# Kernel optimization log

Measured on AMD Instinct MI355X. Metric: run time of the kernel, lower is better.

The kernel has to match this reference:

```python
import jax, jax.numpy as jnp
import numpy as np

HIDDEN = 2048
N_HEADS = 32
N_KV = 8
HEAD_DIM = 64
ROPE_THETA = 10000.0


def setup_inputs() -> dict:
    key = jax.random.key(0)
    k0, k1, k2, k3, k4 = jax.random.split(key, 5)
    B, S = 2, 2048
    scale_in = 1.0 / np.sqrt(HIDDEN)
    return {
        "hidden_states": jax.random.normal(k0, (B, S, HIDDEN), dtype=jnp.float32),
        # weights stored [in, out] (transpose of torch Linear.weight)
        "Wq": jax.random.normal(k1, (HIDDEN, N_HEADS * HEAD_DIM), dtype=jnp.float32) * scale_in,
        "Wk": jax.random.normal(k2, (HIDDEN, N_KV * HEAD_DIM), dtype=jnp.float32) * scale_in,
        "Wv": jax.random.normal(k3, (HIDDEN, N_KV * HEAD_DIM), dtype=jnp.float32) * scale_in,
        "Wo": jax.random.normal(k4, (N_HEADS * HEAD_DIM, HIDDEN), dtype=jnp.float32) * scale_in,
    }


def _rope_tables(seq_len, dim, theta):
    inv_freq = 1.0 / (theta ** (jnp.arange(0, dim, 2, dtype=jnp.float32) / dim))
    t = jnp.arange(seq_len, dtype=jnp.float32)
    freqs = jnp.outer(t, inv_freq)              # [S, D/2]
    emb = jnp.concatenate([freqs, freqs], -1)   # [S, D]
    return jnp.cos(emb), jnp.sin(emb)


def _rotate_half(x):
    d = x.shape[-1] // 2
    return jnp.concatenate([-x[..., d:], x[..., :d]], axis=-1)


def reference(hidden_states, Wq, Wk, Wv, Wo):
    B, S, _ = hidden_states.shape
    G = N_HEADS // N_KV  # groups per kv head

    q = (hidden_states @ Wq).reshape(B, S, N_HEADS, HEAD_DIM).transpose(0, 2, 1, 3)  # [B,H,S,D]
    k = (hidden_states @ Wk).reshape(B, S, N_KV, HEAD_DIM).transpose(0, 2, 1, 3)     # [B,KV,S,D]
    v = (hidden_states @ Wv).reshape(B, S, N_KV, HEAD_DIM).transpose(0, 2, 1, 3)

    cos, sin = _rope_tables(S, HEAD_DIM, ROPE_THETA)  # [S,D]
    q = q * cos + _rotate_half(q) * sin
    k = k * cos + _rotate_half(k) * sin

    # GQA without materializing repeated KV: fold q heads into [KV, G]
    qg = q.reshape(B, N_KV, G, S, HEAD_DIM)
    scale = HEAD_DIM ** -0.5
    scores = jnp.einsum("bkgsd,bktd->bkgst", qg, k) * scale  # [B,KV,G,S,S]

    causal = jnp.tril(jnp.ones((S, S), dtype=bool))
    scores = jnp.where(causal, scores, jnp.float32(-1e30))
    probs = jax.nn.softmax(scores, axis=-1)

    out = jnp.einsum("bkgst,bktd->bkgsd", probs, v)          # [B,KV,G,S,D]
    out = out.reshape(B, N_HEADS, S, HEAD_DIM).transpose(0, 2, 1, 3).reshape(B, S, N_HEADS * HEAD_DIM)
    return out @ Wo
```

## Files before the change

### kernel.cpp

```cpp
#include <hip/hip_runtime.h>
#include <cstdint>
#include <cstddef>

typedef __attribute__((ext_vector_type(8))) short short8;
typedef __attribute__((ext_vector_type(4))) float f32x4;
typedef __attribute__((ext_vector_type(16))) float f32x16;

#define MFMA16(a, b, c) __builtin_amdgcn_mfma_f32_16x16x32_bf16((a), (b), (c), 0, 0, 0)
#define MFMA32(a, b, c) __builtin_amdgcn_mfma_f32_32x32x16_bf16((a), (b), (c), 0, 0, 0)

union F2U { float f; unsigned int u; };
union U4S8 { uint4 u4; unsigned short s[8]; short8 v; };

__device__ __forceinline__ unsigned short f2bf(float f) {
  F2U x; x.f = f;
  unsigned int r = x.u + 0x7fffu + ((x.u >> 16) & 1u);
  return (unsigned short)(r >> 16);
}
__device__ __forceinline__ float bf2f(unsigned short s) {
  F2U x; x.u = ((unsigned int)s) << 16;
  return x.f;
}
__device__ __forceinline__ float fexp2(float x) {
  float r; asm("v_exp_f32 %0, %1" : "=v"(r) : "v"(x)); return r;
}
__device__ __forceinline__ unsigned int cvtpk(float lo, float hiv) {
  unsigned int r; asm("v_cvt_pk_bf16_f32 %0, %1, %2" : "=v"(r) : "v"(lo), "v"(hiv)); return r;
}

#define HIDDEN 2048
#define NHEADS 32
#define NKV 8
#define HDIM 64
#define SEQ 2048
#define BATCH 2
#define NTOK (BATCH * SEQ)
#define QKVN 3072
#define QSCALE 0.18033688011117309f

__global__ __launch_bounds__(256) void rope_table_kernel(float* __restrict__ ct, float* __restrict__ st) {
  int idx = blockIdx.x * 256 + threadIdx.x;
  int s = idx >> 5;
  int i = idx & 31;
  float invf = expf(-(float)i * (9.210340371976184f / 32.0f));
  float f = (float)s * invf;
  ct[idx] = cosf(f);
  st[idx] = sinf(f);
}

__global__ __launch_bounds__(256) void convert_x_kernel(const float* __restrict__ X,
                                                        unsigned short* __restrict__ Xb) {
  size_t i = ((size_t)blockIdx.x * 256 + threadIdx.x) * 8;
  float4 a0 = *(const float4*)(X + i);
  float4 a1 = *(const float4*)(X + i + 4);
  U4S8 p;
  p.s[0] = f2bf(a0.x); p.s[1] = f2bf(a0.y); p.s[2] = f2bf(a0.z); p.s[3] = f2bf(a0.w);
  p.s[4] = f2bf(a1.x); p.s[5] = f2bf(a1.y); p.s[6] = f2bf(a1.z); p.s[7] = f2bf(a1.w);
  *(short8*)(Xb + i) = p.v;
}

__global__ __launch_bounds__(256) void transpose_w_kernel(const float* __restrict__ W,
                                                          unsigned short* __restrict__ Wt,
                                                          int N, int row_off) {
  __shared__ unsigned short lt[64][72];
  const int t = threadIdx.x;
  const int k0 = blockIdx.y * 64, n0 = blockIdx.x * 64;
  #pragma unroll
  for (int p = 0; p < 4; ++p) {
    int kr = p * 16 + (t >> 4);
    int nc = (t & 15) * 4;
    float4 v = *(const float4*)&W[(size_t)(k0 + kr) * N + n0 + nc];
    lt[nc + 0][kr] = f2bf(v.x);
    lt[nc + 1][kr] = f2bf(v.y);
    lt[nc + 2][kr] = f2bf(v.z);
    lt[nc + 3][kr] = f2bf(v.w);
  }
  __syncthreads();
  #pragma unroll
  for (int p = 0; p < 2; ++p) {
    int nr = p * 32 + (t >> 3);
    int kc = (t & 7) * 8;
    *(short8*)&Wt[(size_t)(row_off + n0 + nr) * HIDDEN + k0 + kc] = *(const short8*)&lt[nr][kc];
  }
}

template<int MODE>
__global__ __launch_bounds__(256) void gemm128_kernel(const unsigned short* __restrict__ Ab,
                                                      const unsigned short* __restrict__ Bt,
                                                      void* __restrict__ Cp,
                                                      int M, int N, int K,
                                                      const float* __restrict__ ct,
                                                      const float* __restrict__ st) {
  __shared__ __align__(16) unsigned short lds_a[128][64];
  __shared__ __align__(16) unsigned short lds_b[128][64];

  const int t = threadIdx.x, lane = t & 63, w = t >> 6;
  const int lr = lane & 15, lh = lane >> 4;

  const int orig = blockIdx.y * gridDim.x + blockIdx.x;
  const int nwg  = (int)(gridDim.x * gridDim.y);
  const int cpx  = nwg >> 3;
  const int swz  = (orig & 7) * cpx + (orig >> 3);
  const int m0 = (swz / (int)gridDim.x) * 128;
  const int n0 = (swz % (int)gridDim.x) * 128;

  const int wr = (w >> 1) * 64, wc = (w & 1) * 64;

  f32x4 acc[4][4] = {};

  for (int k0 = 0; k0 < K; k0 += 64) {
    __syncthreads();
    #pragma unroll
    for (int c = 0; c < 4; ++c) {
      int row = w * 32 + c * 8 + (lane >> 3);
      int cks = (lane & 7) ^ (row & 7);
      __builtin_amdgcn_global_load_lds(
          (const __attribute__((address_space(1))) unsigned int*)(Ab + (size_t)(m0 + row) * K + k0 + cks * 8),
          (__attribute__((address_space(3))) unsigned int*)&lds_a[w * 32 + c * 8][0], 16, 0, 0);
      __builtin_amdgcn_global_load_lds(
          (const __attribute__((address_space(1))) unsigned int*)(Bt + (size_t)(n0 + row) * K + k0 + cks * 8),
          (__attribute__((address_space(3))) unsigned int*)&lds_b[w * 32 + c * 8][0], 16, 0, 0);
    }
    __syncthreads();

    #pragma unroll
    for (int kk = 0; kk < 2; ++kk) {
      short8 af[4], bf[4];
      #pragma unroll
      for (int i = 0; i < 4; ++i) {
        int row = wr + i * 16 + lr;
        af[i] = *(const short8*)((const char*)&lds_a[0][0] + row * 128 + (((kk * 4 + lh) ^ (row & 7)) * 16));
      }
      #pragma unroll
      for (int j = 0; j < 4; ++j) {
        int row = wc + j * 16 + lr;
        bf[j] = *(const short8*)((const char*)&lds_b[0][0] + row * 128 + (((kk * 4 + lh) ^ (row & 7)) * 16));
      }
      #pragma unroll
      for (int i = 0; i < 4; ++i)
        #pragma unroll
        for (int j = 0; j < 4; ++j)
          acc[i][j] = MFMA16(af[i], bf[j], acc[i][j]);
    }
  }

  if constexpr (MODE == 0) {
    #pragma unroll
    for (int i = 0; i < 4; ++i)
      #pragma unroll
      for (int j = 0; j < 4; ++j)
        #pragma unroll
        for (int r = 0; r < 4; ++r) {
          int row = m0 + wr + i * 16 + lh * 4 + r;
          int col = n0 + wc + j * 16 + lr;
          ((float*)Cp)[(size_t)row * N + col] = acc[i][j][r];
        }
  } else {
    const bool isV = (n0 >= 2560);
    const bool isQ = (n0 < 2048);
    #pragma unroll
    for (int i = 0; i < 4; ++i)
      #pragma unroll
      for (int r = 0; r < 4; ++r) {
        int row = m0 + wr + i * 16 + lh * 4 + r;
        int s_tok = row & (SEQ - 1);
        float c0 = 0.f, s0 = 0.f, c1 = 0.f, s1 = 0.f;
        if (!isV) {
          c0 = ct[s_tok * 32 + lr];      s0 = st[s_tok * 32 + lr];
          c1 = ct[s_tok * 32 + 16 + lr]; s1 = st[s_tok * 32 + 16 + lr];
        }
        #pragma unroll
        for (int j = 0; j < 4; ++j) {
          int col = n0 + wc + j * 16 + lr;
          float v = acc[i][j][r];
          float o;
          if (isV) {
            o = v;
          } else {
            float p = acc[i][j ^ 2][r];
            float cc = (j & 1) ? c1 : c0;
            float ss = (j & 1) ? s1 : s0;
            o = v * cc + ((j & 2) ? p : -p) * ss;
            if (isQ) o *= QSCALE;
          }
          ((unsigned short*)Cp)[(size_t)row * N + col] = f2bf(o);
        }
      }
  }
}

__global__ __launch_bounds__(256) void v_pack_kernel(const unsigned short* __restrict__ QKV,
                                                     unsigned short* __restrict__ Vt) {
  int idx = blockIdx.x * 256 + threadIdx.x;
  int m = idx >> 9;
  int c = idx & 511;
  int b = m >> 11, s = m & 2047;
  int kv = c >> 6, d = c & 63;
  Vt[(((size_t)(b * NKV + kv)) * HDIM + d) * SEQ + s] = QKV[(size_t)m * QKVN + 2560 + c];
}

#define KVBLK 64

__global__ __launch_bounds__(256, 4) void flash_kernel(const unsigned short* __restrict__ QKV,
                                                       const unsigned short* __restrict__ Vt,
                                                       unsigned short* __restrict__ Ob) {
  const int bx = blockIdx.x;
  const int h = blockIdx.y;
  const int b = blockIdx.z;
  const int kv = h >> 2;
  const int t = threadIdx.x;
  const int lane = t & 63;
  const int w = t >> 6;
  const int q = lane & 31;
  const int hi = lane >> 5;

  __shared__ __align__(16) char smem[32768];
  unsigned short* Klds = (unsigned short*)smem;
  unsigned short* Vlds = (unsigned short*)(smem + 16384);

  const unsigned short* Kg = QKV + (size_t)b * SEQ * QKVN + 2048 + kv * 64;
  const unsigned short* Vg = Vt + ((size_t)(b * NKV + kv)) * HDIM * SEQ;
  const unsigned short* Qh = QKV + (size_t)b * SEQ * QKVN + h * 64;

  const int srow = w * 16 + (lane >> 3);
  const int scks = (lane & 7) ^ (srow & 7);
  const unsigned short* Ksrc = Kg + (size_t)srow * QKVN + scks * 8;
  const unsigned short* Vsrc = Vg + (size_t)srow * SEQ + scks * 8;

  #define STAGE_KV(buf, kt0)                                                              \
    do {                                                                                  \
      __builtin_amdgcn_global_load_lds(                                                   \
          (const __attribute__((address_space(1))) unsigned int*)(Ksrc + (size_t)(kt0) * QKVN), \
          (__attribute__((address_space(3))) unsigned int*)(Klds + (buf) * 4096 + w * 1024), 16, 0, 0); \
      __builtin_amdgcn_global_load_lds(                                                   \
          (const __attribute__((address_space(1))) unsigned int*)(Ksrc + (size_t)(kt0) * QKVN + 8 * QKVN), \
          (__attribute__((address_space(3))) unsigned int*)(Klds + (buf) * 4096 + w * 1024 + 512), 16, 0, 0); \
      __builtin_amdgcn_global_load_lds(                                                   \
          (const __attribute__((address_space(1))) unsigned int*)(Vsrc + (kt0)),          \
          (__attribute__((address_space(3))) unsigned int*)(Vlds + (buf) * 4096 + w * 1024), 16, 0, 0); \
      __builtin_amdgcn_global_load_lds(                                                   \
          (const __attribute__((address_space(1))) unsigned int*)(Vsrc + (kt0) + 8 * SEQ), \
          (__attribute__((address_space(3))) unsigned int*)(Vlds + (buf) * 4096 + w * 1024 + 512), 16, 0, 0); \
    } while (0)

  #pragma unroll 1
  for (int seg = 0; seg < 2; ++seg) {
    const int qb = seg ? bx : (15 - bx);
    const int wq0 = qb * 128 + w * 32;

    short8 qf[4];
    #pragma unroll
    for (int f = 0; f < 4; ++f)
      qf[f] = *(const short8*)&Qh[(size_t)(wq0 + q) * QKVN + f * 16 + hi * 8];

    f32x16 o0 = {}, o1 = {};
    float m_run = -1e30f, l_run = 0.f;

    const int nt_blk = qb * 2 + 2;
    const int nt_w   = qb * 2 + (w >> 1) + 1;

    __syncthreads();
    STAGE_KV(0, 0);
    __syncthreads();
    int cur = 0;

    for (int tt = 0; tt < nt_blk; ++tt) {
      if (tt + 1 < nt_blk) STAGE_KV(cur ^ 1, (tt + 1) * KVBLK);

      if (tt < nt_w) {
        const int kt0 = tt * KVBLK;
        const unsigned short* Kt = Klds + cur * 4096;
        const unsigned short* Vl = Vlds + cur * 4096;

        #pragma unroll
        for (int hk = 0; hk < 2; ++hk) {
          const int kbase = kt0 + hk * 32;
          if (kbase <= wq0 + 31) {
            f32x16 s = {};
            __builtin_amdgcn_s_setprio(1);
            #pragma unroll
            for (int f = 0; f < 4; ++f) {
              short8 kf = *(const short8*)(Kt + (hk * 32 + q) * 64 + (((f * 2 + hi) ^ (q & 7)) * 8));
              s = MFMA32(kf, qf[f], s);
            }
            __builtin_amdgcn_s_setprio(0);

            if (kbase + 31 > wq0) {
              #pragma unroll
              for (int r = 0; r < 16; ++r) {
                int kl = (r & 3) + 8 * (r >> 2) + 4 * hi;
                if (kbase + kl > wq0 + q) s[r] = -1e30f;
              }
            }

            float mt = -1e30f;
            #pragma unroll
            for (int r = 0; r < 16; ++r) mt = fmaxf(mt, s[r]);
            mt = fmaxf(mt, __shfl_xor(mt, 32, 64));

            const bool resc = __any(mt > m_run + 11.0f);
            if (resc) {
              float mn = fmaxf(m_run, mt);
              float alpha = fexp2(m_run - mn);
              m_run = mn;
              l_run *= alpha;
              #pragma unroll
              for (int r = 0; r < 16; ++r) { o0[r] *= alpha; o1[r] *= alpha; }
            }
            float ls = 0.f;
            #pragma unroll
            for (int r = 0; r < 16; ++r) {
              float p = fexp2(s[r] - m_run);
              s[r] = p;
              ls += p;
            }
            ls += __shfl_xor(ls, 32, 64);
            l_run += ls;

            unsigned int own[8], rcv[8];
            #pragma unroll
            for (int g = 0; g < 8; ++g)
              own[g] = cvtpk(s[2 * g], s[2 * g + 1]);
            #pragma unroll
            for (int g = 0; g < 8; ++g)
              rcv[g] = (unsigned int)__shfl_xor((int)own[g], 32, 64);

            __builtin_amdgcn_s_setprio(1);
            {
              U4S8 pfv;
              pfv.u4.x = hi ? rcv[2] : own[0];
              pfv.u4.y = hi ? rcv[3] : own[1];
              pfv.u4.z = hi ? own[2] : rcv[0];
              pfv.u4.w = hi ? own[3] : rcv[1];
              int co = ((hk * 4 + hi) ^ (q & 7)) * 8;
              short8 vf0 = *(const short8*)(Vl + q * 64 + co);
              short8 vf1 = *(const short8*)(Vl + (32 + q) * 64 + co);
              o0 = MFMA32(vf0, pfv.v, o0);
              o1 = MFMA32(vf1, pfv.v, o1);
            }
            {
              U4S8 pfv;
              pfv.u4.x = hi ? rcv[6] : own[4];
              pfv.u4.y = hi ? rcv[7] : own[5];
              pfv.u4.z = hi ? own[6] : rcv[4];
              pfv.u4.w = hi ? own[7] : rcv[5];
              int co = ((hk * 4 + 2 + hi) ^ (q & 7)) * 8;
              short8 vf0 = *(const short8*)(Vl + q * 64 + co);
              short8 vf1 = *(const short8*)(Vl + (32 + q) * 64 + co);
              o0 = MFMA32(vf0, pfv.v, o0);
              o1 = MFMA32(vf1, pfv.v, o1);
            }
            __builtin_amdgcn_s_setprio(0);
          }
        }
      }

      __syncthreads();
      cur ^= 1;
    }

    unsigned short* lo = (unsigned short*)smem + (size_t)w * 32 * 72;
    float inv = 1.0f / l_run;
    #pragma unroll
    for (int gg = 0; gg < 8; ++gg) {
      int r = 2 * gg;
      int dl = (r & 3) + 8 * (r >> 2) + 4 * hi;
      unsigned int w0 = (unsigned int)f2bf(o0[r] * inv) | ((unsigned int)f2bf(o0[r + 1] * inv) << 16);
      unsigned int w1 = (unsigned int)f2bf(o1[r] * inv) | ((unsigned int)f2bf(o1[r + 1] * inv) << 16);
      *(unsigned int*)&lo[q * 72 + dl] = w0;
      *(unsigned int*)&lo[q * 72 + 32 + dl] = w1;
    }
    {
      int row = lane >> 1;
      int ch = (lane & 1) * 32;
      uint4 x0 = *(const uint4*)&lo[row * 72 + ch + 0];
      uint4 x1 = *(const uint4*)&lo[row * 72 + ch + 8];
      uint4 x2 = *(const uint4*)&lo[row * 72 + ch + 16];
      uint4 x3 = *(const uint4*)&lo[row * 72 + ch + 24];
      unsigned short* dst = &Ob[(size_t)(b * SEQ + wq0 + row) * (NHEADS * HDIM) + h * HDIM + ch];
      *(uint4*)(dst + 0)  = x0;
      *(uint4*)(dst + 8)  = x1;
      *(uint4*)(dst + 16) = x2;
      *(uint4*)(dst + 24) = x3;
    }
  }
}

extern "C" void kernel_launch(void* const* d_in, const int* in_sizes, int n_in,
                              void* d_out, int out_size, void* d_ws, size_t ws_size,
                              hipStream_t stream) {
  const float* X  = (const float*)d_in[0];
  const float* Wq = (const float*)d_in[1];
  const float* Wk = (const float*)d_in[2];
  const float* Wv = (const float*)d_in[3];
  const float* Wo = (const float*)d_in[4];
  float* out = (float*)d_out;

  char* ws = (char*)d_ws;
  size_t off = 0;
  auto carve = [&](size_t bytes) -> void* {
    void* p = ws + off;
    off += (bytes + 255) & ~(size_t)255;
    return p;
  };
  float* rope_cos = (float*)carve((size_t)SEQ * 32 * 4);
  float* rope_sin = (float*)carve((size_t)SEQ * 32 * 4);
  unsigned short* Xb     = (unsigned short*)carve((size_t)NTOK * HIDDEN * 2);
  unsigned short* Wqkv_t = (unsigned short*)carve((size_t)QKVN * HIDDEN * 2);
  unsigned short* Wot    = (unsigned short*)carve((size_t)HIDDEN * HIDDEN * 2);
  unsigned short* QKVb   = (unsigned short*)carve((size_t)NTOK * QKVN * 2);
  unsigned short* Vt     = (unsigned short*)carve((size_t)BATCH * NKV * HDIM * SEQ * 2);
  unsigned short* Ob     = Xb;

  rope_table_kernel<<<dim3(256), dim3(256), 0, stream>>>(rope_cos, rope_sin);
  convert_x_kernel<<<dim3((NTOK * HIDDEN) / (256 * 8)), dim3(256), 0, stream>>>(X, Xb);

  transpose_w_kernel<<<dim3(2048 / 64, HIDDEN / 64), dim3(256), 0, stream>>>(Wq, Wqkv_t, 2048, 0);
  transpose_w_kernel<<<dim3(512 / 64,  HIDDEN / 64), dim3(256), 0, stream>>>(Wk, Wqkv_t, 512, 2048);
  transpose_w_kernel<<<dim3(512 / 64,  HIDDEN / 64), dim3(256), 0, stream>>>(Wv, Wqkv_t, 512, 2560);
  transpose_w_kernel<<<dim3(2048 / 64, HIDDEN / 64), dim3(256), 0, stream>>>(Wo, Wot, 2048, 0);

  gemm128_kernel<1><<<dim3(QKVN / 128, NTOK / 128), dim3(256), 0, stream>>>(
      Xb, Wqkv_t, QKVb, NTOK, QKVN, HIDDEN, rope_cos, rope_sin);

  v_pack_kernel<<<dim3((NTOK * NKV * HDIM) / 256), dim3(256), 0, stream>>>(QKVb, Vt);

  flash_kernel<<<dim3(8, NHEADS, BATCH), dim3(256), 0, stream>>>(QKVb, Vt, Ob);

  gemm128_kernel<0><<<dim3(HIDDEN / 128, NTOK / 128), dim3(256), 0, stream>>>(
      Ob, Wot, out, NTOK, HIDDEN, HIDDEN, nullptr, nullptr);
}
```

Before: 226.0 us.

## Split KV tiles across wave pairs in flash kernel and merge partial softmax

The flash attention block grows from 4 to 8 waves. Each pair of waves shares a 32-row query slice, and each wave of the pair handles one 32-key half of every 64-key tile. Partial max, sum and output accumulators are combined through shared memory at the end. This doubles the waves working on the same KV staging, aiming to raise occupancy and hide latency within the causal attention loop. In exchange it adds an LDS reduction step with extra barriers and a larger block, and launch_bounds(512,4) may tighten the register limit.

Result: no change. 222.3 us (-1.6%).

```diff
diff --git a/kernel.cpp b/kernel.cpp
--- a/kernel.cpp
+++ b/kernel.cpp
@@ -201,7 +201,7 @@
 
 #define KVBLK 64
 
-__global__ __launch_bounds__(256, 4) void flash_kernel(const unsigned short* __restrict__ QKV,
+__global__ __launch_bounds__(512, 4) void flash_kernel(const unsigned short* __restrict__ QKV,
                                                        const unsigned short* __restrict__ Vt,
                                                        unsigned short* __restrict__ Ob) {
   const int bx = blockIdx.x;
@@ -211,18 +211,21 @@
   const int t = threadIdx.x;
   const int lane = t & 63;
   const int w = t >> 6;
+  const int p = w >> 1;
+  const int kh = w & 1;
   const int q = lane & 31;
   const int hi = lane >> 5;
 
-  __shared__ __align__(16) char smem[32768];
+  __shared__ __align__(16) char smem[34816];
   unsigned short* Klds = (unsigned short*)smem;
   unsigned short* Vlds = (unsigned short*)(smem + 16384);
+  float* mlArea = (float*)(smem + 32768);
 
   const unsigned short* Kg = QKV + (size_t)b * SEQ * QKVN + 2048 + kv * 64;
   const unsigned short* Vg = Vt + ((size_t)(b * NKV + kv)) * HDIM * SEQ;
   const unsigned short* Qh = QKV + (size_t)b * SEQ * QKVN + h * 64;
 
-  const int srow = w * 16 + (lane >> 3);
+  const int srow = w * 8 + (lane >> 3);
   const int scks = (lane & 7) ^ (srow & 7);
   const unsigned short* Ksrc = Kg + (size_t)srow * QKVN + scks * 8;
   const unsigned short* Vsrc = Vg + (size_t)srow * SEQ + scks * 8;
@@ -231,22 +234,16 @@
     do {                                                                                  \
       __builtin_amdgcn_global_load_lds(                                                   \
           (const __attribute__((address_space(1))) unsigned int*)(Ksrc + (size_t)(kt0) * QKVN), \
-          (__attribute__((address_space(3))) unsigned int*)(Klds + (buf) * 4096 + w * 1024), 16, 0, 0); \
-      __builtin_amdgcn_global_load_lds(                                                   \
-          (const __attribute__((address_space(1))) unsigned int*)(Ksrc + (size_t)(kt0) * QKVN + 8 * QKVN), \
-          (__attribute__((address_space(3))) unsigned int*)(Klds + (buf) * 4096 + w * 1024 + 512), 16, 0, 0); \
+          (__attribute__((address_space(3))) unsigned int*)(Klds + (buf) * 4096 + w * 512), 16, 0, 0); \
       __builtin_amdgcn_global_load_lds(                                                   \
           (const __attribute__((address_space(1))) unsigned int*)(Vsrc + (kt0)),          \
-          (__attribute__((address_space(3))) unsigned int*)(Vlds + (buf) * 4096 + w * 1024), 16, 0, 0); \
-      __builtin_amdgcn_global_load_lds(                                                   \
-          (const __attribute__((address_space(1))) unsigned int*)(Vsrc + (kt0) + 8 * SEQ), \
-          (__attribute__((address_space(3))) unsigned int*)(Vlds + (buf) * 4096 + w * 1024 + 512), 16, 0, 0); \
+          (__attribute__((address_space(3))) unsigned int*)(Vlds + (buf) * 4096 + w * 512), 16, 0, 0); \
     } while (0)
 
   #pragma unroll 1
   for (int seg = 0; seg < 2; ++seg) {
     const int qb = seg ? bx : (15 - bx);
-    const int wq0 = qb * 128 + w * 32;
+    const int wq0 = qb * 128 + p * 32;
 
     short8 qf[4];
     #pragma unroll
@@ -257,7 +254,6 @@
     float m_run = -1e30f, l_run = 0.f;
 
     const int nt_blk = qb * 2 + 2;
-    const int nt_w   = qb * 2 + (w >> 1) + 1;
 
     __syncthreads();
     STAGE_KV(0, 0);
@@ -267,121 +263,145 @@
     for (int tt = 0; tt < nt_blk; ++tt) {
       if (tt + 1 < nt_blk) STAGE_KV(cur ^ 1, (tt + 1) * KVBLK);
 
-      if (tt < nt_w) {
-        const int kt0 = tt * KVBLK;
+      const int kbase = tt * KVBLK + kh * 32;
+      if (kbase <= wq0 + 31) {
         const unsigned short* Kt = Klds + cur * 4096;
         const unsigned short* Vl = Vlds + cur * 4096;
 
-        #pragma unroll
-        for (int hk = 0; hk < 2; ++hk) {
-          const int kbase = kt0 + hk * 32;
-          if (kbase <= wq0 + 31) {
-            f32x16 s = {};
-            __builtin_amdgcn_s_setprio(1);
-            #pragma unroll
-            for (int f = 0; f < 4; ++f) {
-              short8 kf = *(const short8*)(Kt + (hk * 32 + q) * 64 + (((f * 2 + hi) ^ (q & 7)) * 8));
-              s = MFMA32(kf, qf[f], s);
-            }
-            __builtin_amdgcn_s_setprio(0);
-
-            if (kbase + 31 > wq0) {
-              #pragma unroll
-              for (int r = 0; r < 16; ++r) {
-                int kl = (r & 3) + 8 * (r >> 2) + 4 * hi;
-                if (kbase + kl > wq0 + q) s[r] = -1e30f;
-              }
-            }
-
-            float mt = -1e30f;
-            #pragma unroll
-            for (int r = 0; r < 16; ++r) mt = fmaxf(mt, s[r]);
-            mt = fmaxf(mt, __shfl_xor(mt, 32, 64));
-
-            const bool resc = __any(mt > m_run + 11.0f);
-            if (resc) {
-              float mn = fmaxf(m_run, mt);
-              float alpha = fexp2(m_run - mn);
-              m_run = mn;
-              l_run *= alpha;
-              #pragma unroll
-              for (int r = 0; r < 16; ++r) { o0[r] *= alpha; o1[r] *= alpha; }
-            }
-            float ls = 0.f;
-            #pragma unroll
-            for (int r = 0; r < 16; ++r) {
-              float p = fexp2(s[r] - m_run);
-              s[r] = p;
-              ls += p;
-            }
-            ls += __shfl_xor(ls, 32, 64);
-            l_run += ls;
-
-            unsigned int own[8], rcv[8];
-            #pragma unroll
-            for (int g = 0; g < 8; ++g)
-              own[g] = cvtpk(s[2 * g], s[2 * g + 1]);
-            #pragma unroll
-            for (int g = 0; g < 8; ++g)
-              rcv[g] = (unsigned int)__shfl_xor((int)own[g], 32, 64);
-
-            __builtin_amdgcn_s_setprio(1);
-            {
-              U4S8 pfv;
-              pfv.u4.x = hi ? rcv[2] : own[0];
-              pfv.u4.y = hi ? rcv[3] : own[1];
-              pfv.u4.z = hi ? own[2] : rcv[0];
-              pfv.u4.w = hi ? own[3] : rcv[1];
-              int co = ((hk * 4 + hi) ^ (q & 7)) * 8;
-              short8 vf0 = *(const short8*)(Vl + q * 64 + co);
-              short8 vf1 = *(const short8*)(Vl + (32 + q) * 64 + co);
-              o0 = MFMA32(vf0, pfv.v, o0);
-              o1 = MFMA32(vf1, pfv.v, o1);
-            }
-            {
-              U4S8 pfv;
-              pfv.u4.x = hi ? rcv[6] : own[4];
-              pfv.u4.y = hi ? rcv[7] : own[5];
-              pfv.u4.z = hi ? own[6] : rcv[4];
-              pfv.u4.w = hi ? own[7] : rcv[5];
-              int co = ((hk * 4 + 2 + hi) ^ (q & 7)) * 8;
-              short8 vf0 = *(const short8*)(Vl + q * 64 + co);
-              short8 vf1 = *(const short8*)(Vl + (32 + q) * 64 + co);
-              o0 = MFMA32(vf0, pfv.v, o0);
-              o1 = MFMA32(vf1, pfv.v, o1);
-            }
-            __builtin_amdgcn_s_setprio(0);
+        f32x16 s = {};
+        __builtin_amdgcn_s_setprio(1);
+        #pragma unroll
+        for (int f = 0; f < 4; ++f) {
+          short8 kf = *(const short8*)(Kt + (kh * 32 + q) * 64 + (((f * 2 + hi) ^ (q & 7)) * 8));
+          s = MFMA32(kf, qf[f], s);
+        }
+        __builtin_amdgcn_s_setprio(0);
+
+        if (kbase + 31 > wq0) {
+          #pragma unroll
+          for (int r = 0; r < 16; ++r) {
+            int kl = (r & 3) + 8 * (r >> 2) + 4 * hi;
+            if (kbase + kl > wq0 + q) s[r] = -1e30f;
           }
         }
+
+        float mt = -1e30f;
+        #pragma unroll
+        for (int r = 0; r < 16; ++r) mt = fmaxf(mt, s[r]);
+        mt = fmaxf(mt, __shfl_xor(mt, 32, 64));
+
+        const bool resc = __any(mt > m_run + 11.0f);
+        if (resc) {
+          float mn = fmaxf(m_run, mt);
+          float alpha = fexp2(m_run - mn);
+          m_run = mn;
+          l_run *= alpha;
+          #pragma unroll
+          for (int r = 0; r < 16; ++r) { o0[r] *= alpha; o1[r] *= alpha; }
+        }
+        float ls = 0.f;
+        #pragma unroll
+        for (int r = 0; r < 16; ++r) {
+          float pp = fexp2(s[r] - m_run);
+          s[r] = pp;
+          ls += pp;
+        }
+        ls += __shfl_xor(ls, 32, 64);
+        l_run += ls;
+
+        unsigned int own[8], rcv[8];
+        #pragma unroll
+        for (int g = 0; g < 8; ++g)
+          own[g] = cvtpk(s[2 * g], s[2 * g + 1]);
+        #pragma unroll
+        for (int g = 0; g < 8; ++g)
+          rcv[g] = (unsigned int)__shfl_xor((int)own[g], 32, 64);
+
+        __builtin_amdgcn_s_setprio(1);
+        {
+          U4S8 pfv;
+          pfv.u4.x = hi ? rcv[2] : own[0];
+          pfv.u4.y = hi ? rcv[3] : own[1];
+          pfv.u4.z = hi ? own[2] : rcv[0];
+          pfv.u4.w = hi ? own[3] : rcv[1];
+          int co = ((kh * 4 + hi) ^ (q & 7)) * 8;
+          short8 vf0 = *(const short8*)(Vl + q * 64 + co);
+          short8 vf1 = *(const short8*)(Vl + (32 + q) * 64 + co);
+          o0 = MFMA32(vf0, pfv.v, o0);
+          o1 = MFMA32(vf1, pfv.v, o1);
+        }
+        {
+          U4S8 pfv;
+          pfv.u4.x = hi ? rcv[6] : own[4];
+          pfv.u4.y = hi ? rcv[7] : own[5];
+          pfv.u4.z = hi ? own[6] : rcv[4];
+          pfv.u4.w = hi ? own[7] : rcv[5];
+          int co = ((kh * 4 + 2 + hi) ^ (q & 7)) * 8;
+          short8 vf0 = *(const short8*)(Vl + q * 64 + co);
+          short8 vf1 = *(const short8*)(Vl + (32 + q) * 64 + co);
+          o0 = MFMA32(vf0, pfv.v, o0);
+          o1 = MFMA32(vf1, pfv.v, o1);
+        }
+        __builtin_amdgcn_s_setprio(0);
       }
 
       __syncthreads();
       cur ^= 1;
     }
 
-    unsigned short* lo = (unsigned short*)smem + (size_t)w * 32 * 72;
-    float inv = 1.0f / l_run;
-    #pragma unroll
-    for (int gg = 0; gg < 8; ++gg) {
-      int r = 2 * gg;
-      int dl = (r & 3) + 8 * (r >> 2) + 4 * hi;
-      unsigned int w0 = (unsigned int)f2bf(o0[r] * inv) | ((unsigned int)f2bf(o0[r + 1] * inv) << 16);
-      unsigned int w1 = (unsigned int)f2bf(o1[r] * inv) | ((unsigned int)f2bf(o1[r + 1] * inv) << 16);
-      *(unsigned int*)&lo[q * 72 + dl] = w0;
-      *(unsigned int*)&lo[q * 72 + 32 + dl] = w1;
-    }
-    {
-      int row = lane >> 1;
-      int ch = (lane & 1) * 32;
-      uint4 x0 = *(const uint4*)&lo[row * 72 + ch + 0];
-      uint4 x1 = *(const uint4*)&lo[row * 72 + ch + 8];
-      uint4 x2 = *(const uint4*)&lo[row * 72 + ch + 16];
-      uint4 x3 = *(const uint4*)&lo[row * 72 + ch + 24];
-      unsigned short* dst = &Ob[(size_t)(b * SEQ + wq0 + row) * (NHEADS * HDIM) + h * HDIM + ch];
-      *(uint4*)(dst + 0)  = x0;
-      *(uint4*)(dst + 8)  = x1;
-      *(uint4*)(dst + 16) = x2;
-      *(uint4*)(dst + 24) = x3;
+    if (hi == 0) {
+      mlArea[(w * 32 + q) * 2 + 0] = m_run;
+      mlArea[(w * 32 + q) * 2 + 1] = l_run;
+    }
+    __syncthreads();
+    const int wo = p * 2 + (kh ^ 1);
+    float m_oth = mlArea[(wo * 32 + q) * 2 + 0];
+    float l_oth = mlArea[(wo * 32 + q) * 2 + 1];
+    float m_tot = fmaxf(m_run, m_oth);
+    float alf = fexp2(m_run - m_tot);
+    float l_tot = l_run * alf + l_oth * fexp2(m_oth - m_tot);
+    #pragma unroll
+    for (int r = 0; r < 16; ++r) { o0[r] *= alf; o1[r] *= alf; }
+
+    float* oArea = (float*)smem + (size_t)p * 2048;
+    if (kh == 1) {
+      float* dst = oArea + lane * 32;
+      #pragma unroll
+      for (int r = 0; r < 16; ++r) { dst[r] = o0[r]; dst[16 + r] = o1[r]; }
+    }
+    __syncthreads();
+    if (kh == 0) {
+      const float* src = oArea + lane * 32;
+      #pragma unroll
+      for (int r = 0; r < 16; ++r) { o0[r] += src[r]; o1[r] += src[16 + r]; }
+    }
+    __syncthreads();
+
+    if (kh == 0) {
+      unsigned short* lo = (unsigned short*)smem + (size_t)p * 2304;
+      float inv = 1.0f / l_tot;
+      #pragma unroll
+      for (int gg = 0; gg < 8; ++gg) {
+        int r = 2 * gg;
+        int dl = (r & 3) + 8 * (r >> 2) + 4 * hi;
+        unsigned int w0 = (unsigned int)f2bf(o0[r] * inv) | ((unsigned int)f2bf(o0[r + 1] * inv) << 16);
+        unsigned int w1 = (unsigned int)f2bf(o1[r] * inv) | ((unsigned int)f2bf(o1[r + 1] * inv) << 16);
+        *(unsigned int*)&lo[q * 72 + dl] = w0;
+        *(unsigned int*)&lo[q * 72 + 32 + dl] = w1;
+      }
+      {
+        int row = lane >> 1;
+        int ch = (lane & 1) * 32;
+        uint4 x0 = *(const uint4*)&lo[row * 72 + ch + 0];
+        uint4 x1 = *(const uint4*)&lo[row * 72 + ch + 8];
+        uint4 x2 = *(const uint4*)&lo[row * 72 + ch + 16];
+        uint4 x3 = *(const uint4*)&lo[row * 72 + ch + 24];
+        unsigned short* dst = &Ob[(size_t)(b * SEQ + wq0 + row) * (NHEADS * HDIM) + h * HDIM + ch];
+        *(uint4*)(dst + 0)  = x0;
+        *(uint4*)(dst + 8)  = x1;
+        *(uint4*)(dst + 16) = x2;
+        *(uint4*)(dst + 24) = x3;
+      }
     }
   }
 }
@@ -425,7 +445,7 @@
 
   v_pack_kernel<<<dim3((NTOK * NKV * HDIM) / 256), dim3(256), 0, stream>>>(QKVb, Vt);
 
-  flash_kernel<<<dim3(8, NHEADS, BATCH), dim3(256), 0, stream>>>(QKVb, Vt, Ob);
+  flash_kernel<<<dim3(8, NHEADS, BATCH), dim3(512), 0, stream>>>(QKVb, Vt, Ob);
 
   gemm128_kernel<0><<<dim3(HIDDEN / 128, NTOK / 128), dim3(256), 0, stream>>>(
       Ob, Wot, out, NTOK, HIDDEN, HIDDEN, nullptr, nullptr);
```
